# Kernel optimization log

Measured on AMD Instinct MI355X. Metric: run time of the kernel, lower is better.

## Reference

```python
import jax, jax.numpy as jnp
import numpy as np

B, S, E, H = 2, 2048, 1024, 16
D = E // H  # head_dim = 64


def setup_inputs() -> dict:
    key = jax.random.key(0)
    ks = jax.random.split(key, 6)
    sc = 0.02
    return {
        "hidden_states": jax.random.normal(ks[0], (B, S, E), dtype=jnp.float32),
        "attn_bias": jax.random.normal(ks[1], (S, S), dtype=jnp.float32) * sc,
        "Wqkv": jax.random.normal(ks[2], (E, 3 * E), dtype=jnp.float32) * sc,
        "bqkv": jax.random.normal(ks[3], (3 * E,), dtype=jnp.float32) * sc,
        "Wproj": jax.random.normal(ks[4], (E, E), dtype=jnp.float32) * sc,
        "bproj": jax.random.normal(ks[5], (E,), dtype=jnp.float32) * sc,
    }


def reference(hidden_states, attn_bias, Wqkv, bqkv, Wproj, bproj):
    b, s, e = hidden_states.shape
    qkv = hidden_states @ Wqkv + bqkv                      # [b,s,3e]
    q, k, v = jnp.split(qkv, 3, axis=-1)                   # each [b,s,e]
    cache_key, cache_value = k, v                          # kvCache
    # [b,h,s,d]
    qh = q.reshape(b, s, H, D).transpose(0, 2, 1, 3)
    kh = k.reshape(b, s, H, D).transpose(0, 2, 1, 3)
    vh = v.reshape(b, s, H, D).transpose(0, 2, 1, 3)
    scores = jnp.einsum("bhqd,bhkd->bhqk", qh, kh) / jnp.sqrt(jnp.float32(D))
    scores = scores + attn_bias[:s, :s][None, None]        # learned additive bias
    causal = jnp.tril(jnp.ones((s, s), dtype=bool))
    scores = jnp.where(causal[None, None], scores, jnp.float32(-1e9))
    attn = jax.nn.softmax(scores, axis=-1)
    ctx = jnp.einsum("bhqk,bhkd->bhqd", attn, vh)
    ctx = ctx.transpose(0, 2, 1, 3).reshape(b, s, e)
    out = ctx @ Wproj + bproj                              # resid dropout p=0 -> identity
    return (out, cache_key, cache_value)
```

## Files before the change

### kernel.cpp

```cpp
#include <hip/hip_runtime.h>

#define B_ 2
#define S_ 2048
#define E_ 1024
#define H_ 16
#define D_ 64

typedef short  s16x8 __attribute__((ext_vector_type(8)));
typedef float  f32x4 __attribute__((ext_vector_type(4)));
typedef unsigned short u16x4 __attribute__((ext_vector_type(4)));

__device__ __forceinline__ ushort f2bf(float f) {
    union { float f; unsigned u; } x; x.f = f;
    unsigned u = x.u + 0x7fffu + ((x.u >> 16) & 1u);
    return (ushort)(u >> 16);
}

__global__ __launch_bounds__(256) void cvtx_kernel(
    const float* __restrict__ X, ushort* __restrict__ Xbf)
{
    int i = (blockIdx.x * 256 + threadIdx.x) * 4;
    float4 v = *(const float4*)&X[i];
    u16x4 o;
    o.x = f2bf(v.x); o.y = f2bf(v.y); o.z = f2bf(v.z); o.w = f2bf(v.w);
    *(u16x4*)&Xbf[i] = o;
}

__global__ __launch_bounds__(256) void wtrans_kernel(
    const float* __restrict__ W, ushort* __restrict__ Wt, int Kdim, int Ndim)
{
    __shared__ float tile[64][65];
    int n0 = blockIdx.x * 64, k0 = blockIdx.y * 64;
    int tid = threadIdx.x;
    int c = tid & 63;
#pragma unroll
    for (int r = tid >> 6; r < 64; r += 4)
        tile[r][c] = W[(size_t)(k0 + r) * Ndim + n0 + c];
    __syncthreads();
#pragma unroll
    for (int r = tid >> 6; r < 64; r += 4)
        Wt[(size_t)(n0 + r) * Kdim + k0 + c] = f2bf(tile[c][r]);
}

__global__ __launch_bounds__(256) void gemm_mfma_bt(
    const ushort* __restrict__ A,
    const ushort* __restrict__ Bt,
    const float* __restrict__ bias,
    int M, int N, int K,
    float* __restrict__ C0,
    ushort* __restrict__ Qbf, float* __restrict__ Kf32, ushort* __restrict__ Kbf,
    float* __restrict__ Vf32, int mode)
{
    __shared__ ushort As[128 * 32];
    __shared__ ushort Bs[128 * 32];
    int tid = threadIdx.x;
    int wid = tid >> 6, lane = tid & 63;
    int l15 = lane & 15, quad = lane >> 4;
    int wm = wid >> 1, wn = wid & 1;
    int row0 = blockIdx.y * 128, col0 = blockIdx.x * 128;

    int sr = wid * 16 + (lane >> 2);
    int sk = (lane & 3) * 8;

    f32x4 acc[4][4];
#pragma unroll
    for (int mt = 0; mt < 4; mt++)
#pragma unroll
        for (int nt = 0; nt < 4; nt++) acc[mt][nt] = (f32x4){0.f, 0.f, 0.f, 0.f};

    for (int k0 = 0; k0 < K; k0 += 32) {
        __syncthreads();
#pragma unroll
        for (int c = 0; c < 2; c++) {
            int r = c * 64 + sr;
            __builtin_amdgcn_global_load_lds(
                (const __attribute__((address_space(1))) unsigned int*)
                    &A[(size_t)(row0 + r) * K + k0 + sk],
                (__attribute__((address_space(3))) unsigned int*)&As[r * 32 + sk],
                16, 0, 0);
            __builtin_amdgcn_global_load_lds(
                (const __attribute__((address_space(1))) unsigned int*)
                    &Bt[(size_t)(col0 + r) * K + k0 + sk],
                (__attribute__((address_space(3))) unsigned int*)&Bs[r * 32 + sk],
                16, 0, 0);
        }
        __syncthreads();

        s16x8 af[4], bf[4];
#pragma unroll
        for (int mt = 0; mt < 4; mt++)
            af[mt] = *(const s16x8*)&As[(wm * 64 + mt * 16 + l15) * 32 + quad * 8];
#pragma unroll
        for (int nt = 0; nt < 4; nt++)
            bf[nt] = *(const s16x8*)&Bs[(wn * 64 + nt * 16 + l15) * 32 + quad * 8];
#pragma unroll
        for (int mt = 0; mt < 4; mt++)
#pragma unroll
            for (int nt = 0; nt < 4; nt++)
                acc[mt][nt] = __builtin_amdgcn_mfma_f32_16x16x32_bf16(
                    af[mt], bf[nt], acc[mt][nt], 0, 0, 0);
    }

#pragma unroll
    for (int nt = 0; nt < 4; nt++) {
        int n = col0 + wn * 64 + nt * 16 + l15;
        float bv = bias[n];
        if (mode == 1) {
            int seg = n >> 10;
            int nn = n & (E_ - 1);
#pragma unroll
            for (int mt = 0; mt < 4; mt++)
#pragma unroll
                for (int r = 0; r < 4; r++) {
                    int row = row0 + wm * 64 + mt * 16 + quad * 4 + r;
                    float v = acc[mt][nt][r] + bv;
                    size_t idx = (size_t)row * E_ + nn;
                    if (seg == 0)      Qbf[idx] = f2bf(v);
                    else if (seg == 1) { Kf32[idx] = v; Kbf[idx] = f2bf(v); }
                    else               Vf32[idx] = v;
                }
        } else {
#pragma unroll
            for (int mt = 0; mt < 4; mt++)
#pragma unroll
                for (int r = 0; r < 4; r++) {
                    int row = row0 + wm * 64 + mt * 16 + quad * 4 + r;
                    C0[(size_t)row * N + n] = acc[mt][nt][r] + bv;
                }
        }
    }
}

__global__ __launch_bounds__(256) void vtrans_kernel(
    const float* __restrict__ V, ushort* __restrict__ Vt)
{
    __shared__ float tile[64][65];
    int blk = blockIdx.x;
    int s0 = (blk & 31) * 64;
    int bh = blk >> 5;
    int b = bh >> 4, h = bh & 15;
    int tid = threadIdx.x;
    int d = tid & 63;
#pragma unroll
    for (int i = tid >> 6; i < 64; i += 4)
        tile[i][d] = V[((size_t)(b * S_ + s0 + i)) * E_ + h * 64 + d];
    __syncthreads();
    int lane = tid & 63, w = tid >> 6;
#pragma unroll
    for (int dd = w; dd < 64; dd += 4)
        Vt[((size_t)(bh * 64 + dd)) * S_ + s0 + lane] = f2bf(tile[lane][dd]);
}

__global__ __launch_bounds__(256) void attn_mfma_kernel(
    const ushort* __restrict__ Qbf,
    const ushort* __restrict__ Kbf,
    const ushort* __restrict__ Vt,
    const float* __restrict__ bias,
    ushort* __restrict__ Ctx)
{
    __shared__ ushort Ks[64][72];
    __shared__ ushort Vs[64][72];
    __shared__ ushort Ps[4][16][72];

    int blk = blockIdx.x;
    int bh = blk & 31;
    int qt = 31 - (blk >> 5);
    int b = bh >> 4, h = bh & 15;
    int tid = threadIdx.x;
    int wid = tid >> 6, lane = tid & 63;
    int l15 = lane & 15, quad = lane >> 4;

    int skey = tid >> 2;
    int scol = (tid & 3) * 16;
    const float scale = 0.125f;

    const size_t krow = (size_t)(b * S_ + skey) * E_ + h * 64 + scol;
    const size_t vrow = (size_t)(bh * 64 + skey) * S_ + scol;

    int q0w = qt * 64 + wid * 16;

    const size_t qbase = ((size_t)(b * S_ + q0w + l15)) * E_ + h * 64 + quad * 8;
    s16x8 qa0 = *(const s16x8*)&Qbf[qbase];
    s16x8 qa1 = *(const s16x8*)&Qbf[qbase + 32];

    f32x4 o[4];
#pragma unroll
    for (int dt = 0; dt < 4; dt++) o[dt] = (f32x4){0.f, 0.f, 0.f, 0.f};
    float lsum[4];
#pragma unroll
    for (int r = 0; r < 4; r++) lsum[r] = 0.f;

    float4 kr0 = ((const float4*)&Kbf[krow])[0];
    float4 kr1 = ((const float4*)&Kbf[krow])[1];
    float4 vr0 = ((const float4*)&Vt[vrow])[0];
    float4 vr1 = ((const float4*)&Vt[vrow])[1];
    float bvn[4][4];
#pragma unroll
    for (int r = 0; r < 4; r++)
#pragma unroll
        for (int kt = 0; kt < 4; kt++)
            bvn[r][kt] = bias[(size_t)(q0w + quad * 4 + r) * S_ + kt * 16 + l15];

    for (int t = 0; t <= qt; t++) {
        int j0 = t * 64;
        __syncthreads();
        *(float4*)&Ks[skey][scol]     = kr0;
        *(float4*)&Ks[skey][scol + 8] = kr1;
        *(float4*)&Vs[skey][scol]     = vr0;
        *(float4*)&Vs[skey][scol + 8] = vr1;
        float bv[4][4];
#pragma unroll
        for (int r = 0; r < 4; r++)
#pragma unroll
            for (int kt = 0; kt < 4; kt++) bv[r][kt] = bvn[r][kt];
        __syncthreads();

        if (t < qt) {
            int j1 = j0 + 64;
            kr0 = ((const float4*)&Kbf[krow + (size_t)j1 * E_])[0];
            kr1 = ((const float4*)&Kbf[krow + (size_t)j1 * E_])[1];
            vr0 = ((const float4*)&Vt[vrow + j1])[0];
            vr1 = ((const float4*)&Vt[vrow + j1])[1];
#pragma unroll
            for (int r = 0; r < 4; r++)
#pragma unroll
                for (int kt = 0; kt < 4; kt++)
                    bvn[r][kt] = bias[(size_t)(q0w + quad * 4 + r) * S_ + j1 + kt * 16 + l15];
        }

        f32x4 s[4];
#pragma unroll
        for (int kt = 0; kt < 4; kt++) {
            s16x8 kb0 = *(const s16x8*)&Ks[kt * 16 + l15][quad * 8];
            s16x8 kb1 = *(const s16x8*)&Ks[kt * 16 + l15][quad * 8 + 32];
            f32x4 acc = (f32x4){0.f, 0.f, 0.f, 0.f};
            acc = __builtin_amdgcn_mfma_f32_16x16x32_bf16(qa0, kb0, acc, 0, 0, 0);
            acc = __builtin_amdgcn_mfma_f32_16x16x32_bf16(qa1, kb1, acc, 0, 0, 0);
            s[kt] = acc;
        }

        bool diag = (t == qt);
#pragma unroll
        for (int r = 0; r < 4; r++) {
            int row = q0w + quad * 4 + r;
#pragma unroll
            for (int kt = 0; kt < 4; kt++) {
                int j = j0 + kt * 16 + l15;
                float v = s[kt][r] * scale + bv[r][kt];
                float p = (diag && j > row) ? 0.f : __expf(v);
                lsum[r] += p;
                int chunk = (kt * 2 + (l15 >> 3)) ^ quad;
                Ps[wid][quad * 4 + r][chunk * 8 + (l15 & 7)] = f2bf(p);
            }
        }

        int cb = (quad ^ (l15 >> 2)) * 8;
        s16x8 pa0 = *(const s16x8*)&Ps[wid][l15][cb];
        s16x8 pa1 = *(const s16x8*)&Ps[wid][l15][cb + 32];
#pragma unroll
        for (int dt = 0; dt < 4; dt++) {
            s16x8 vb0 = *(const s16x8*)&Vs[dt * 16 + l15][quad * 8];
            s16x8 vb1 = *(const s16x8*)&Vs[dt * 16 + l15][quad * 8 + 32];
            o[dt] = __builtin_amdgcn_mfma_f32_16x16x32_bf16(pa0, vb0, o[dt], 0, 0, 0);
            o[dt] = __builtin_amdgcn_mfma_f32_16x16x32_bf16(pa1, vb1, o[dt], 0, 0, 0);
        }
    }

    float inv_l[4];
#pragma unroll
    for (int r = 0; r < 4; r++) {
        float l = lsum[r];
        l += __shfl_xor(l, 1);
        l += __shfl_xor(l, 2);
        l += __shfl_xor(l, 4);
        l += __shfl_xor(l, 8);
        inv_l[r] = 1.f / l;
    }

#pragma unroll
    for (int dt = 0; dt < 4; dt++) {
#pragma unroll
        for (int r = 0; r < 4; r++) {
            int row = q0w + quad * 4 + r;
            Ctx[((size_t)(b * S_ + row)) * E_ + h * 64 + dt * 16 + l15] =
                f2bf(o[dt][r] * inv_l[r]);
        }
    }
}

extern "C" void kernel_launch(void* const* d_in, const int* in_sizes, int n_in,
                              void* d_out, int out_size, void* d_ws, size_t ws_size,
                              hipStream_t stream) {
    const float* X     = (const float*)d_in[0];
    const float* abias = (const float*)d_in[1];
    const float* Wqkv  = (const float*)d_in[2];
    const float* bqkv  = (const float*)d_in[3];
    const float* Wproj = (const float*)d_in[4];
    const float* bproj = (const float*)d_in[5];

    const size_t plane = (size_t)B_ * S_ * E_;
    float* out  = (float*)d_out;
    float* kout = out + plane;
    float* vout = kout + plane;

    ushort* xbf    = (ushort*)d_ws;
    ushort* qbf    = xbf + plane;
    ushort* kbf    = qbf + plane;
    ushort* vt     = kbf + plane;
    ushort* ctxbf  = xbf;
    ushort* wqkvt  = vt + plane;
    ushort* wprojt = wqkvt + (size_t)3 * E_ * E_;

    const int M = B_ * S_;

    cvtx_kernel<<<dim3(plane / 1024), 256, 0, stream>>>(X, xbf);
    wtrans_kernel<<<dim3(3 * E_ / 64, E_ / 64), 256, 0, stream>>>(Wqkv, wqkvt, E_, 3 * E_);
    wtrans_kernel<<<dim3(E_ / 64, E_ / 64), 256, 0, stream>>>(Wproj, wprojt, E_, E_);

    gemm_mfma_bt<<<dim3(3 * E_ / 128, M / 128), 256, 0, stream>>>(
        xbf, wqkvt, bqkv, M, 3 * E_, E_,
        nullptr, qbf, kout, kbf, vout, 1);

    vtrans_kernel<<<dim3(B_ * H_ * (S_ / 64)), 256, 0, stream>>>(vout, vt);

    attn_mfma_kernel<<<dim3(B_ * H_ * 32), 256, 0, stream>>>(
        qbf, kbf, vt, abias, ctxbf);

    gemm_mfma_bt<<<dim3(E_ / 128, M / 128), 256, 0, stream>>>(
        ctxbf, wprojt, bproj, M, E_, E_,
        out, nullptr, nullptr, nullptr, nullptr, 0);
}
```

Before: 239.2 us.

## Load K/V fragments directly from global memory, drop LDS staging and block barriers

The attention kernel no longer stages K and V tiles through shared memory with two __syncthreads per iteration. Each wave now loads its MFMA operand fragments straight from global memory (through L2/cache), and the software prefetch of the next tile is dropped. The block-to-(bh, q-tile) mapping is also reordered so that groups of 8 heads run together, which should improve L2 reuse of K, V and bias. The cost is that each of the 4 waves in a block now issues the same K/V reads separately (4x redundant global traffic), and the loads are no longer explicitly overlapped with compute.

```diff
diff --git a/kernel.cpp b/kernel.cpp
--- a/kernel.cpp
+++ b/kernel.cpp
@@ -158,24 +158,18 @@
     const float* __restrict__ bias,
     ushort* __restrict__ Ctx)
 {
-    __shared__ ushort Ks[64][72];
-    __shared__ ushort Vs[64][72];
     __shared__ ushort Ps[4][16][72];
 
     int blk = blockIdx.x;
-    int bh = blk & 31;
-    int qt = 31 - (blk >> 5);
+    int x  = blk & 7;
+    int g  = blk >> 3;
+    int bh = x + 8 * (g & 3);
+    int qt = 31 - (g >> 2);
     int b = bh >> 4, h = bh & 15;
     int tid = threadIdx.x;
     int wid = tid >> 6, lane = tid & 63;
     int l15 = lane & 15, quad = lane >> 4;
-
-    int skey = tid >> 2;
-    int scol = (tid & 3) * 16;
     const float scale = 0.125f;
-
-    const size_t krow = (size_t)(b * S_ + skey) * E_ + h * 64 + scol;
-    const size_t vrow = (size_t)(bh * 64 + skey) * S_ + scol;
 
     int q0w = qt * 64 + wid * 16;
 
@@ -183,6 +177,10 @@
     s16x8 qa0 = *(const s16x8*)&Qbf[qbase];
     s16x8 qa1 = *(const s16x8*)&Qbf[qbase + 32];
 
+    const ushort* kbase = &Kbf[(size_t)(b * S_ + l15) * E_ + h * 64 + quad * 8];
+    const ushort* vbase = &Vt[(size_t)(bh * 64 + l15) * S_ + quad * 8];
+    const float*  bbase = &bias[(size_t)(q0w + quad * 4) * S_ + l15];
+
     f32x4 o[4];
 #pragma unroll
     for (int dt = 0; dt < 4; dt++) o[dt] = (f32x4){0.f, 0.f, 0.f, 0.f};
@@ -190,52 +188,38 @@
 #pragma unroll
     for (int r = 0; r < 4; r++) lsum[r] = 0.f;
 
-    float4 kr0 = ((const float4*)&Kbf[krow])[0];
-    float4 kr1 = ((const float4*)&Kbf[krow])[1];
-    float4 vr0 = ((const float4*)&Vt[vrow])[0];
-    float4 vr1 = ((const float4*)&Vt[vrow])[1];
-    float bvn[4][4];
-#pragma unroll
-    for (int r = 0; r < 4; r++)
-#pragma unroll
-        for (int kt = 0; kt < 4; kt++)
-            bvn[r][kt] = bias[(size_t)(q0w + quad * 4 + r) * S_ + kt * 16 + l15];
-
     for (int t = 0; t <= qt; t++) {
         int j0 = t * 64;
-        __syncthreads();
-        *(float4*)&Ks[skey][scol]     = kr0;
-        *(float4*)&Ks[skey][scol + 8] = kr1;
-        *(float4*)&Vs[skey][scol]     = vr0;
-        *(float4*)&Vs[skey][scol + 8] = vr1;
+
         float bv[4][4];
 #pragma unroll
         for (int r = 0; r < 4; r++)
 #pragma unroll
-            for (int kt = 0; kt < 4; kt++) bv[r][kt] = bvn[r][kt];
-        __syncthreads();
-
-        if (t < qt) {
-            int j1 = j0 + 64;
-            kr0 = ((const float4*)&Kbf[krow + (size_t)j1 * E_])[0];
-            kr1 = ((const float4*)&Kbf[krow + (size_t)j1 * E_])[1];
-            vr0 = ((const float4*)&Vt[vrow + j1])[0];
-            vr1 = ((const float4*)&Vt[vrow + j1])[1];
-#pragma unroll
-            for (int r = 0; r < 4; r++)
-#pragma unroll
-                for (int kt = 0; kt < 4; kt++)
-                    bvn[r][kt] = bias[(size_t)(q0w + quad * 4 + r) * S_ + j1 + kt * 16 + l15];
+            for (int kt = 0; kt < 4; kt++)
+                bv[r][kt] = bbase[(size_t)r * S_ + j0 + kt * 16];
+
+        s16x8 kb0[4], kb1[4];
+#pragma unroll
+        for (int kt = 0; kt < 4; kt++) {
+            const ushort* kp = &kbase[(size_t)(j0 + kt * 16) * E_];
+            kb0[kt] = *(const s16x8*)kp;
+            kb1[kt] = *(const s16x8*)(kp + 32);
+        }
+
+        s16x8 vb0[4], vb1[4];
+#pragma unroll
+        for (int dt = 0; dt < 4; dt++) {
+            const ushort* vp = &vbase[(size_t)(dt * 16) * S_ + j0];
+            vb0[dt] = *(const s16x8*)vp;
+            vb1[dt] = *(const s16x8*)(vp + 32);
         }
 
         f32x4 s[4];
 #pragma unroll
         for (int kt = 0; kt < 4; kt++) {
-            s16x8 kb0 = *(const s16x8*)&Ks[kt * 16 + l15][quad * 8];
-            s16x8 kb1 = *(const s16x8*)&Ks[kt * 16 + l15][quad * 8 + 32];
             f32x4 acc = (f32x4){0.f, 0.f, 0.f, 0.f};
-            acc = __builtin_amdgcn_mfma_f32_16x16x32_bf16(qa0, kb0, acc, 0, 0, 0);
-            acc = __builtin_amdgcn_mfma_f32_16x16x32_bf16(qa1, kb1, acc, 0, 0, 0);
+            acc = __builtin_amdgcn_mfma_f32_16x16x32_bf16(qa0, kb0[kt], acc, 0, 0, 0);
+            acc = __builtin_amdgcn_mfma_f32_16x16x32_bf16(qa1, kb1[kt], acc, 0, 0, 0);
             s[kt] = acc;
         }
 
@@ -259,10 +243,8 @@
         s16x8 pa1 = *(const s16x8*)&Ps[wid][l15][cb + 32];
 #pragma unroll
         for (int dt = 0; dt < 4; dt++) {
-            s16x8 vb0 = *(const s16x8*)&Vs[dt * 16 + l15][quad * 8];
-            s16x8 vb1 = *(const s16x8*)&Vs[dt * 16 + l15][quad * 8 + 32];
-            o[dt] = __builtin_amdgcn_mfma_f32_16x16x32_bf16(pa0, vb0, o[dt], 0, 0, 0);
-            o[dt] = __builtin_amdgcn_mfma_f32_16x16x32_bf16(pa1, vb1, o[dt], 0, 0, 0);
+            o[dt] = __builtin_amdgcn_mfma_f32_16x16x32_bf16(pa0, vb0[dt], o[dt], 0, 0, 0);
+            o[dt] = __builtin_amdgcn_mfma_f32_16x16x32_bf16(pa1, vb1[dt], o[dt], 0, 0, 0);
         }
     }
 
```

Result: slower. 328.3 us (+37.2%).
